# Kernel tuning notes

Measured on AMD Instinct MI355X. Metric: run time of the kernel, lower is better.

## Reference

```python
import jax, jax.numpy as jnp
import numpy as np

K_MASK = -2.3819763e+38
NUM_HEADS = 16
NUM_KV_HEADS = 8
FEATURES = 2048
HEAD_DIM = 128
WINDOW = 1024
SOFT_CAP = 50.0
B, T = 2, 2048


def apply_rope(inputs, positions, head_dim, max_wavelength=10000):
    # inputs: [B, T, N, H], positions: [B, T]
    fraction = 2 * jnp.arange(0, head_dim // 2) / head_dim
    timescale = max_wavelength ** fraction
    sinusoid_inp = positions[..., None] / timescale[None, None, :]  # [B,T,H/2]
    sinusoid_inp = sinusoid_inp[..., None, :]  # [B,T,1,H/2]
    sin = jnp.sin(sinusoid_inp)
    cos = jnp.cos(sinusoid_inp)
    first_half, second_half = jnp.split(inputs, 2, axis=-1)
    first_part = first_half * cos - second_half * sin
    second_part = second_half * cos + first_half * sin
    return jnp.concatenate([first_part, second_part], axis=-1).astype(inputs.dtype)


def setup_inputs() -> dict:
    key = jax.random.key(0)
    k1, k2, k3, k4 = jax.random.split(key, 4)
    std = 0.02
    x = jax.random.normal(k1, (B, T, FEATURES), dtype=jnp.float32)
    segment_pos = jnp.broadcast_to(jnp.arange(T, dtype=jnp.int32), (B, T))
    # causal prefill mask [B, T, T]
    attn_mask = jnp.broadcast_to(jnp.tril(jnp.ones((T, T), dtype=bool)), (B, T, T))
    wq = jax.random.normal(k2, (NUM_HEADS, FEATURES, HEAD_DIM), dtype=jnp.float32) * std
    wkv = jax.random.normal(k3, (2, NUM_KV_HEADS, FEATURES, HEAD_DIM), dtype=jnp.float32) * std
    wo = jax.random.normal(k4, (NUM_HEADS, HEAD_DIM, FEATURES), dtype=jnp.float32) * std
    return {"x": x, "segment_pos": segment_pos, "attn_mask": attn_mask,
            "wq": wq, "wkv": wkv, "wo": wo}


def reference(x, segment_pos, attn_mask, wq, wkv, wo):
    # Projections (GQA path: num_kv_heads != num_heads)
    q = jnp.einsum('BTD,NDH->BTNH', x, wq)              # [B,T,N,H]
    k = jnp.einsum('BSD,KDH->BSKH', x, wkv[0])          # [B,S,K,H]
    v = jnp.einsum('BSD,KDH->BSKH', x, wkv[1])          # [B,S,K,H]

    q = apply_rope(q, segment_pos, HEAD_DIM)
    q = q * HEAD_DIM ** (-0.5)
    k = apply_rope(k, segment_pos, HEAD_DIM)

    b, t, n, h = q.shape
    g = n // NUM_KV_HEADS
    qg = q.reshape(b, t, NUM_KV_HEADS, g, h)
    logits = jnp.einsum('BTKGH,BSKH->BTKGS', qg, k)
    s = logits.shape[-1]
    logits = logits.reshape(b, t, n, s)

    # soft cap
    logits = jnp.tanh(logits / SOFT_CAP) * SOFT_CAP

    # sliding-window mask combined with attn_mask
    cache_positions = jnp.arange(s)[None, None, :]
    sp = segment_pos[:, :, None]
    sliding_mask = (cache_positions >= sp - WINDOW + 1) & (cache_positions <= sp + WINDOW - 1)
    mask = sliding_mask & attn_mask  # [B,T,S]

    padded_logits = jnp.where(mask[:, :, None, :], logits, K_MASK)
    probs = jax.nn.softmax(padded_logits, axis=-1).astype(k.dtype)

    pg = probs.reshape(b, t, NUM_KV_HEADS, g, s)
    encoded = jnp.einsum('BTKGS,BSKH->BTKGH', pg, v).reshape(b, t, n, h)
    attn_output = jnp.einsum('BTNH,NHD->BTD', encoded, wo)
    return attn_output
```

## Files before the change

kernel.cpp:

```cpp
#include <hip/hip_runtime.h>

typedef unsigned short u16;
typedef unsigned int u32;
typedef __attribute__((ext_vector_type(8))) short bfx8;
typedef __attribute__((ext_vector_type(4))) float fx4;

static __device__ __forceinline__ float b2f(u16 u) {
    union { float f; u32 i; } c; c.i = ((u32)u) << 16; return c.f;
}
static __device__ __forceinline__ u16 f2b(float f) {
    union { float f; u32 i; } c; c.f = f;
    u32 r = c.i + 0x7FFFu + ((c.i >> 16) & 1u);
    return (u16)(r >> 16);
}
typedef const __attribute__((address_space(1))) unsigned int* gas1;
typedef __attribute__((address_space(3))) unsigned int* las3;
static __device__ __forceinline__ void gll16(const void* g, void* l) {
    __builtin_amdgcn_global_load_lds((gas1)g, (las3)l, 16, 0, 0);
}

__global__ __launch_bounds__(256) void k_convert_x(const float* __restrict__ x, u16* __restrict__ xb) {
    size_t i = ((size_t)blockIdx.x * 256 + threadIdx.x) * 8;
    float4 a = *(const float4*)(x + i);
    float4 b = *(const float4*)(x + i + 4);
    union { u16 e[8]; uint4 v; } o;
    o.e[0] = f2b(a.x); o.e[1] = f2b(a.y); o.e[2] = f2b(a.z); o.e[3] = f2b(a.w);
    o.e[4] = f2b(b.x); o.e[5] = f2b(b.y); o.e[6] = f2b(b.z); o.e[7] = f2b(b.w);
    *(uint4*)(xb + i) = o.v;
}

__global__ __launch_bounds__(256) void k_pack_w1(const float* __restrict__ wq, const float* __restrict__ wkv,
                                                 u16* __restrict__ wb1) {
    __shared__ float t[128 * 33];
    int ci = blockIdx.x;
    int k0 = blockIdx.y << 5;
    int c0 = ci << 7;
    const float* src;
    if (ci < 16)      src = wq  + (size_t)ci * 2048 * 128;
    else if (ci < 24) src = wkv + (size_t)(ci - 16) * 2048 * 128;
    else              src = wkv + (size_t)(8 + ci - 24) * 2048 * 128;
    int tid = threadIdx.x;
#pragma unroll
    for (int i = 0; i < 16; i++) {
        int idx = i * 256 + tid;
        int kk = idx >> 7, cc = idx & 127;
        t[cc * 33 + kk] = src[(size_t)(k0 + kk) * 128 + cc];
    }
    __syncthreads();
#pragma unroll
    for (int i = 0; i < 16; i++) {
        int idx = i * 256 + tid;
        int cc = idx >> 5, kk = idx & 31;
        wb1[(size_t)(c0 + cc) * 2048 + k0 + kk] = f2b(t[cc * 33 + kk]);
    }
}

__global__ __launch_bounds__(256) void k_pack_w2(const float* __restrict__ wo, u16* __restrict__ wb2) {
    __shared__ float t[128 * 33];
    int c0 = blockIdx.x << 7;
    int k0 = blockIdx.y << 5;
    int tid = threadIdx.x;
#pragma unroll
    for (int i = 0; i < 16; i++) {
        int idx = i * 256 + tid;
        int kk = idx >> 7, cc = idx & 127;
        t[cc * 33 + kk] = wo[(size_t)(k0 + kk) * 2048 + c0 + cc];
    }
    __syncthreads();
#pragma unroll
    for (int i = 0; i < 16; i++) {
        int idx = i * 256 + tid;
        int cc = idx >> 5, kk = idx & 31;
        wb2[(size_t)(c0 + cc) * 2048 + k0 + kk] = f2b(t[cc * 33 + kk]);
    }
}

template <int BM, int OUT_BF16>
__global__ __launch_bounds__(512, 2) void k_gemm256(const u16* __restrict__ A, const u16* __restrict__ Bt,
                                                    void* __restrict__ C, int M, int N, int K) {
    constexpr int MF = BM / 32;
    constexpr int NA = BM / 16;
    constexpr int FR = NA + 16;
    constexpr int LPW = FR / 8;
    __shared__ u16 lds[4 * FR * 512];

    int tid = threadIdx.x, wave = tid >> 6, lane = tid & 63;
    int quad = lane >> 4, l16 = lane & 15;
    int wm = wave >> 2, wn = wave & 3;

    int nwg = gridDim.x * gridDim.y;
    int bid = blockIdx.y * gridDim.x + blockIdx.x;
    int swz = (bid & 7) * (nwg >> 3) + (bid >> 3);
    int bx = swz % gridDim.x, by = swz / gridDim.x;
    int r0 = by * BM, c0 = bx << 8;

    fx4 zero = {0.f, 0.f, 0.f, 0.f};
    fx4 acc[MF][4];
#pragma unroll
    for (int m = 0; m < MF; m++)
#pragma unroll
        for (int n = 0; n < 4; n++) acc[m][n] = zero;

    const u16* gsrc[LPW];
#pragma unroll
    for (int j = 0; j < LPW; j++) {
        int fw = wave * LPW + j;
        gsrc[j] = (fw < NA ? A + (size_t)(r0 + fw * 16 + l16) * K
                           : Bt + (size_t)(c0 + (fw - NA) * 16 + l16) * K) + quad * 8;
    }
    u16* ldst = lds + wave * (LPW * 512);

    int NT = K >> 5;
#pragma unroll
    for (int p = 0; p < 3; p++)
#pragma unroll
        for (int j = 0; j < LPW; j++) gll16(gsrc[j] + p * 32, ldst + p * (FR * 512) + j * 512);

    for (int t = 0; t < NT; ++t) {
        int rem = NT - 1 - t;
        if (rem >= 2)      asm volatile("s_waitcnt vmcnt(%0)" : : "n"(2 * LPW) : "memory");
        else if (rem == 1) asm volatile("s_waitcnt vmcnt(%0)" : : "n"(LPW) : "memory");
        else               asm volatile("s_waitcnt vmcnt(0)" : : : "memory");
        __builtin_amdgcn_s_barrier();

        const u16* Fb = lds + (t & 3) * (FR * 512);
        const u16* Ab = Fb + wm * (MF * 512);
        const u16* Bb = Fb + (NA + wn * 4) * 512;
        bfx8 bf[4], af[4];
#pragma unroll
        for (int n = 0; n < 4; n++) bf[n] = *(const bfx8*)(Bb + n * 512 + lane * 8);
#pragma unroll
        for (int m = 0; m < 4; m++) af[m] = *(const bfx8*)(Ab + m * 512 + lane * 8);
        if (t + 3 < NT) {
            u16* dst = lds + ((t + 3) & 3) * (FR * 512) + wave * (LPW * 512);
#pragma unroll
            for (int j = 0; j < LPW; j++) gll16(gsrc[j] + (size_t)(t + 3) * 32, dst + j * 512);
        }
        __builtin_amdgcn_s_barrier();
        __builtin_amdgcn_s_setprio(1);
#pragma unroll
        for (int m = 0; m < 4; m++)
#pragma unroll
            for (int n = 0; n < 4; n++)
                acc[m][n] = __builtin_amdgcn_mfma_f32_16x16x32_bf16(af[m], bf[n], acc[m][n], 0, 0, 0);
        __builtin_amdgcn_s_setprio(0);
        if constexpr (MF == 8) {
            __builtin_amdgcn_s_barrier();
#pragma unroll
            for (int m = 0; m < 4; m++) af[m] = *(const bfx8*)(Ab + (4 + m) * 512 + lane * 8);
            __builtin_amdgcn_s_barrier();
            __builtin_amdgcn_s_setprio(1);
#pragma unroll
            for (int m = 0; m < 4; m++)
#pragma unroll
                for (int n = 0; n < 4; n++)
                    acc[4 + m][n] = __builtin_amdgcn_mfma_f32_16x16x32_bf16(af[m], bf[n], acc[4 + m][n], 0, 0, 0);
            __builtin_amdgcn_s_setprio(0);
        }
    }
#pragma unroll
    for (int m = 0; m < MF; m++)
#pragma unroll
        for (int n = 0; n < 4; n++) {
            int col = c0 + wn * 64 + n * 16 + l16;
#pragma unroll
            for (int r = 0; r < 4; r++) {
                int row = r0 + wm * (BM / 2) + m * 16 + quad * 4 + r;
                float v = acc[m][n][r];
                if (OUT_BF16) ((u16*)C)[(size_t)row * N + col] = f2b(v);
                else          ((float*)C)[(size_t)row * N + col] = v;
            }
        }
}

__global__ __launch_bounds__(256) void k_rope(const u16* __restrict__ qkv, u16* __restrict__ Qb,
                                              u16* __restrict__ Kb, u16* __restrict__ Vb) {
    __shared__ float sc[128];
    int bt = blockIdx.x;
    int b = bt >> 11, t = bt & 2047;
    const u16* row = qkv + (size_t)bt * 4096;
    int tid = threadIdx.x;
    float tf = (float)t;
    const float RS = 0.08838834764831845f;
    const float LT = 0.20762050593046f;
    if (tid < 64) {
        float ang = tf * exp2f(-LT * (float)tid);
        float s, c; sincosf(ang, &s, &c);
        sc[tid] = s; sc[tid + 64] = c;
    }
    __syncthreads();
#pragma unroll
    for (int i = 0; i < 4; i++) {
        int idx = tid + i * 256;
        int n = idx >> 6, hp = idx & 63;
        float x1 = b2f(row[n * 128 + hp]);
        float x2 = b2f(row[n * 128 + hp + 64]);
        float s = sc[hp], c = sc[hp + 64];
        size_t o = ((size_t)(b * 16 + n) * 2048 + t) * 128 + hp;
        Qb[o]      = f2b((x1 * c - x2 * s) * RS);
        Qb[o + 64] = f2b((x2 * c + x1 * s) * RS);
    }
#pragma unroll
    for (int i = 0; i < 2; i++) {
        int idx = tid + i * 256;
        int kh = idx >> 6, hp = idx & 63;
        float x1 = b2f(row[2048 + kh * 128 + hp]);
        float x2 = b2f(row[2048 + kh * 128 + hp + 64]);
        float s = sc[hp], c = sc[hp + 64];
        size_t o = ((size_t)(b * 8 + kh) * 2048 + t) * 128 + hp;
        Kb[o]      = f2b(x1 * c - x2 * s);
        Kb[o + 64] = f2b(x2 * c + x1 * s);
    }
#pragma unroll
    for (int i = 0; i < 4; i++) {
        int idx = tid + i * 256;
        int kh = idx >> 7, h = idx & 127;
        Vb[((size_t)(b * 8 + kh) * 2048 + t) * 128 + h] = row[3072 + idx];
    }
}

__global__ __launch_bounds__(256) void k_transpose_v(const u16* __restrict__ Vb, u16* __restrict__ Vt) {
    __shared__ u16 t[128 * 136];
    int bk = blockIdx.y;
    int t0 = blockIdx.x << 7;
    const u16* src = Vb + ((size_t)bk * 2048 + t0) * 128;
    u16* dst = Vt + (size_t)bk * 128 * 2048 + t0;
    int tid = threadIdx.x;
#pragma unroll
    for (int it = 0; it < 8; it++) {
        int ch = tid + it * 256;
        int tt = ch >> 4, c8 = (ch & 15) << 3;
        *(uint4*)(t + tt * 136 + c8) = *(const uint4*)(src + (size_t)tt * 128 + c8);
    }
    __syncthreads();
#pragma unroll
    for (int it = 0; it < 8; it++) {
        int ch = tid + it * 256;
        int h = ch >> 4, s8 = (ch & 15) << 3;
        union { uint4 v; u16 e[8]; } vv;
#pragma unroll
        for (int j = 0; j < 8; j++) vv.e[j] = t[(s8 + j) * 136 + h];
        *(uint4*)(dst + (size_t)h * 2048 + s8) = vv.v;
    }
}

__global__ __launch_bounds__(512, 4) void k_attn(const u16* __restrict__ Qb, const u16* __restrict__ Kb,
                                                 const u16* __restrict__ Vt, u16* __restrict__ enc) {
    __shared__ u16 Ks[2][16 * 512];
    __shared__ u16 Vs[2][16 * 512];
    __shared__ u16 Pl[8 * 1024];
    int t0 = blockIdx.x << 6;
    int kh = blockIdx.y, b = blockIdx.z;
    int tid = threadIdx.x, wave = tid >> 6, lane = tid & 63;
    int quad = lane >> 4, l16 = lane & 15;
    int n = (kh << 1) + (wave >> 2);
    int tw = t0 + ((wave & 3) << 4);
    const u16* Qp = Qb + (size_t)(b * 16 + n) * 2048 * 128;
    const u16* Kp = Kb + (size_t)(b * 8 + kh) * 2048 * 128;
    const u16* Vp = Vt + (size_t)(b * 8 + kh) * 128 * 2048;

    bfx8 aq[4];
#pragma unroll
    for (int kb = 0; kb < 4; kb++)
        aq[kb] = *(const bfx8*)(Qp + (size_t)(tw + l16) * 128 + kb * 32 + quad * 8);

    const u16* kgp[2]; const u16* vgp[2];
#pragma unroll
    for (int q = 0; q < 2; q++) {
        int f = wave * 2 + q;
        kgp[q] = Kp + (size_t)((f >> 2) * 16 + l16) * 128 + (f & 3) * 32 + quad * 8;
        vgp[q] = Vp + (size_t)((f >> 1) * 16 + l16) * 2048 + (f & 1) * 32 + quad * 8;
    }
    u16* Pw = Pl + wave * 1024;

    fx4 zero = {0.f, 0.f, 0.f, 0.f};
    fx4 o_acc[8];
#pragma unroll
    for (int hb = 0; hb < 8; hb++) o_acc[hb] = zero;
    float lsum[4] = {0.f, 0.f, 0.f, 0.f};

    const float C1 = 0.057707801635559f;
    const float C2 = 144.269504088896f;

    int s_lo = t0 - 1023; if (s_lo < 0) s_lo = 0;
    int ts0 = s_lo >> 6, ts1 = t0 >> 6;

#pragma unroll
    for (int q = 0; q < 2; q++) {
        int f = wave * 2 + q;
        gll16(kgp[q] + (size_t)(ts0 << 6) * 128, Ks[0] + f * 512);
        gll16(vgp[q] + (ts0 << 6), Vs[0] + f * 512);
    }

    for (int ts = ts0; ts <= ts1; ts++) {
        int cur = (ts - ts0) & 1;
        int s0 = ts << 6;
        __builtin_amdgcn_s_barrier();
        if (ts < ts1) {
            int s1 = (ts + 1) << 6;
#pragma unroll
            for (int q = 0; q < 2; q++) {
                int f = wave * 2 + q;
                gll16(kgp[q] + (size_t)s1 * 128, Ks[cur ^ 1] + f * 512);
                gll16(vgp[q] + s1, Vs[cur ^ 1] + f * 512);
            }
            asm volatile("s_waitcnt vmcnt(4)" : : : "memory");
        } else {
            asm volatile("s_waitcnt vmcnt(0)" : : : "memory");
        }
        __builtin_amdgcn_s_barrier();

        if (s0 <= tw + 15 && s0 + 63 >= tw - 1023) {
            const u16* Kc = Ks[cur];
            const u16* Vc = Vs[cur];
            bool full = (s0 + 63 <= tw) && (s0 >= tw - 1008);
            if (full) {
#pragma unroll
                for (int nb = 0; nb < 4; nb++) {
                    fx4 sacc = zero;
                    __builtin_amdgcn_s_setprio(1);
#pragma unroll
                    for (int kb = 0; kb < 4; kb++) {
                        bfx8 bk = *(const bfx8*)(Kc + (nb * 4 + kb) * 512 + lane * 8);
                        sacc = __builtin_amdgcn_mfma_f32_16x16x32_bf16(aq[kb], bk, sacc, 0, 0, 0);
                    }
                    __builtin_amdgcn_s_setprio(0);
                    int base0 = ((nb >> 1) * 64 + ((nb & 1) * 2 + (l16 >> 3)) * 16 + quad * 4) * 8 + (l16 & 7);
#pragma unroll
                    for (int r = 0; r < 4; r++) {
                        float u = __builtin_amdgcn_exp2f(sacc[r] * C1);
                        float p = __builtin_amdgcn_exp2f(-C2 * __builtin_amdgcn_rcpf(u + 1.f));
                        lsum[r] += p;
                        Pw[base0 + r * 8] = f2b(p);
                    }
                }
            } else {
#pragma unroll
                for (int nb = 0; nb < 4; nb++) {
                    int sb = s0 + (nb << 4);
                    int base0 = ((nb >> 1) * 64 + ((nb & 1) * 2 + (l16 >> 3)) * 16 + quad * 4) * 8 + (l16 & 7);
                    if (sb <= tw + 15 && sb + 15 >= tw - 1023) {
                        fx4 sacc = zero;
#pragma unroll
                        for (int kb = 0; kb < 4; kb++) {
                            bfx8 bk = *(const bfx8*)(Kc + (nb * 4 + kb) * 512 + lane * 8);
                            sacc = __builtin_amdgcn_mfma_f32_16x16x32_bf16(aq[kb], bk, sacc, 0, 0, 0);
                        }
                        int sg = sb + l16;
#pragma unroll
                        for (int r = 0; r < 4; r++) {
                            int tg = tw + quad * 4 + r;
                            float u = __builtin_amdgcn_exp2f(sacc[r] * C1);
                            float p = __builtin_amdgcn_exp2f(-C2 * __builtin_amdgcn_rcpf(u + 1.f));
                            p = (sg <= tg && sg >= tg - 1023) ? p : 0.f;
                            lsum[r] += p;
                            Pw[base0 + r * 8] = f2b(p);
                        }
                    } else {
#pragma unroll
                        for (int r = 0; r < 4; r++) Pw[base0 + r * 8] = 0;
                    }
                }
            }
            asm volatile("s_waitcnt lgkmcnt(0)" : : : "memory");
            __builtin_amdgcn_sched_barrier(0);
            bfx8 pf[2];
#pragma unroll
            for (int kk = 0; kk < 2; kk++)
                pf[kk] = *(const bfx8*)(Pw + kk * 512 + lane * 8);
            __builtin_amdgcn_s_setprio(1);
#pragma unroll
            for (int hb = 0; hb < 8; hb++)
#pragma unroll
                for (int kk = 0; kk < 2; kk++) {
                    bfx8 vf = *(const bfx8*)(Vc + (hb * 2 + kk) * 512 + lane * 8);
                    o_acc[hb] = __builtin_amdgcn_mfma_f32_16x16x32_bf16(pf[kk], vf, o_acc[hb], 0, 0, 0);
                }
            __builtin_amdgcn_s_setprio(0);
        }
    }
#pragma unroll
    for (int r = 0; r < 4; r++) {
#pragma unroll
        for (int off = 1; off < 16; off <<= 1)
            lsum[r] += __shfl_xor(lsum[r], off);
        lsum[r] = 1.0f / lsum[r];
    }
#pragma unroll
    for (int hb = 0; hb < 8; hb++) {
        int h = hb * 16 + l16;
#pragma unroll
        for (int r = 0; r < 4; r++) {
            int tg = tw + quad * 4 + r;
            enc[((size_t)(b * 2048 + tg) * 16 + n) * 128 + h] = f2b(o_acc[hb][r] * lsum[r]);
        }
    }
}

extern "C" void kernel_launch(void* const* d_in, const int* in_sizes, int n_in,
                              void* d_out, int out_size, void* d_ws, size_t ws_size,
                              hipStream_t stream) {
    const float* x   = (const float*)d_in[0];
    const float* wq  = (const float*)d_in[3];
    const float* wkv = (const float*)d_in[4];
    const float* wo  = (const float*)d_in[5];
    char* ws = (char*)d_ws;
    const size_t MiB = 1024 * 1024;
    u16* xb  = (u16*)(ws);
    u16* wb1 = (u16*)(ws + 16 * MiB);
    u16* qkv = (u16*)(ws + 32 * MiB);
    u16* Qb  = (u16*)(ws);
    u16* Kb  = (u16*)(ws + 16 * MiB);
    u16* Vb  = (u16*)(ws + 24 * MiB);
    u16* enc = (u16*)(ws + 32 * MiB);
    u16* wb2 = (u16*)(ws + 48 * MiB);
    u16* Vt  = (u16*)(ws + 56 * MiB);

    k_convert_x<<<4096, 256, 0, stream>>>(x, xb);
    k_pack_w1<<<dim3(32, 64), 256, 0, stream>>>(wq, wkv, wb1);
    k_gemm256<256, 1><<<dim3(16, 16), 512, 0, stream>>>(xb, wb1, qkv, 4096, 4096, 2048);
    k_rope<<<4096, 256, 0, stream>>>(qkv, Qb, Kb, Vb);
    k_transpose_v<<<dim3(16, 16), 256, 0, stream>>>(Vb, Vt);
    k_pack_w2<<<dim3(16, 64), 256, 0, stream>>>(wo, wb2);
    k_attn<<<dim3(32, 8, 2), 512, 0, stream>>>(Qb, Kb, Vt, enc);
    k_gemm256<128, 0><<<dim3(8, 32), 512, 0, stream>>>(enc, wb2, d_out, 4096, 2048, 2048);
}
```

Baseline: 357.5 us.

## Merge prep kernels, restructure GEMM pipeline to 8-phase double buffer, rope Q in place

Merges the x conversion and W1 packing into one launch. Merges rope, V transpose and Wo packing into another. Q is now roped in place inside the qkv buffer and read by attention with a 4096 stride, which removes the separate Qb and Vb copies, and Vt is staged in the output buffer. The GEMM changes from a 4-stage K=32 pipeline to a 2-stage K=64 double buffer with interleaved LDS-read/MFMA phases separated by barriers. The trade-offs are fewer launches and less traffic against a shallower prefetch depth, more barriers, and a strided Q read.

```diff
diff --git a/kernel.cpp b/kernel.cpp
--- a/kernel.cpp
+++ b/kernel.cpp
@@ -19,70 +19,53 @@
     __builtin_amdgcn_global_load_lds((gas1)g, (las3)l, 16, 0, 0);
 }
 
-__global__ __launch_bounds__(256) void k_convert_x(const float* __restrict__ x, u16* __restrict__ xb) {
-    size_t i = ((size_t)blockIdx.x * 256 + threadIdx.x) * 8;
-    float4 a = *(const float4*)(x + i);
-    float4 b = *(const float4*)(x + i + 4);
-    union { u16 e[8]; uint4 v; } o;
-    o.e[0] = f2b(a.x); o.e[1] = f2b(a.y); o.e[2] = f2b(a.z); o.e[3] = f2b(a.w);
-    o.e[4] = f2b(b.x); o.e[5] = f2b(b.y); o.e[6] = f2b(b.z); o.e[7] = f2b(b.w);
-    *(uint4*)(xb + i) = o.v;
-}
-
-__global__ __launch_bounds__(256) void k_pack_w1(const float* __restrict__ wq, const float* __restrict__ wkv,
-                                                 u16* __restrict__ wb1) {
+__global__ __launch_bounds__(256) void k_prep1(const float* __restrict__ x, u16* __restrict__ xb,
+                                               const float* __restrict__ wq, const float* __restrict__ wkv,
+                                               u16* __restrict__ wb1) {
     __shared__ float t[128 * 33];
-    int ci = blockIdx.x;
-    int k0 = blockIdx.y << 5;
+    int bid = blockIdx.x, tid = threadIdx.x;
+    if (bid < 4096) {
+        size_t i = ((size_t)bid * 256 + tid) * 8;
+        float4 a = *(const float4*)(x + i);
+        float4 b = *(const float4*)(x + i + 4);
+        union { u16 e[8]; uint4 v; } o;
+        o.e[0] = f2b(a.x); o.e[1] = f2b(a.y); o.e[2] = f2b(a.z); o.e[3] = f2b(a.w);
+        o.e[4] = f2b(b.x); o.e[5] = f2b(b.y); o.e[6] = f2b(b.z); o.e[7] = f2b(b.w);
+        *(uint4*)(xb + i) = o.v;
+        return;
+    }
+    int idx = bid - 4096;
+    int ci = idx & 31;
+    int k0 = (idx >> 5) << 5;
     int c0 = ci << 7;
     const float* src;
     if (ci < 16)      src = wq  + (size_t)ci * 2048 * 128;
     else if (ci < 24) src = wkv + (size_t)(ci - 16) * 2048 * 128;
     else              src = wkv + (size_t)(8 + ci - 24) * 2048 * 128;
-    int tid = threadIdx.x;
 #pragma unroll
     for (int i = 0; i < 16; i++) {
-        int idx = i * 256 + tid;
-        int kk = idx >> 7, cc = idx & 127;
+        int id2 = i * 256 + tid;
+        int kk = id2 >> 7, cc = id2 & 127;
         t[cc * 33 + kk] = src[(size_t)(k0 + kk) * 128 + cc];
     }
     __syncthreads();
 #pragma unroll
     for (int i = 0; i < 16; i++) {
-        int idx = i * 256 + tid;
-        int cc = idx >> 5, kk = idx & 31;
+        int id2 = i * 256 + tid;
+        int cc = id2 >> 5, kk = id2 & 31;
         wb1[(size_t)(c0 + cc) * 2048 + k0 + kk] = f2b(t[cc * 33 + kk]);
     }
 }
 
-__global__ __launch_bounds__(256) void k_pack_w2(const float* __restrict__ wo, u16* __restrict__ wb2) {
-    __shared__ float t[128 * 33];
-    int c0 = blockIdx.x << 7;
-    int k0 = blockIdx.y << 5;
-    int tid = threadIdx.x;
-#pragma unroll
-    for (int i = 0; i < 16; i++) {
-        int idx = i * 256 + tid;
-        int kk = idx >> 7, cc = idx & 127;
-        t[cc * 33 + kk] = wo[(size_t)(k0 + kk) * 2048 + c0 + cc];
-    }
-    __syncthreads();
-#pragma unroll
-    for (int i = 0; i < 16; i++) {
-        int idx = i * 256 + tid;
-        int cc = idx >> 5, kk = idx & 31;
-        wb2[(size_t)(c0 + cc) * 2048 + k0 + kk] = f2b(t[cc * 33 + kk]);
-    }
-}
-
 template <int BM, int OUT_BF16>
-__global__ __launch_bounds__(512, 2) void k_gemm256(const u16* __restrict__ A, const u16* __restrict__ Bt,
-                                                    void* __restrict__ C, int M, int N, int K) {
+__global__ __launch_bounds__(512, 2) void k_gemm8p(const u16* __restrict__ A, const u16* __restrict__ Bt,
+                                                   void* __restrict__ C, int M, int N, int K) {
     constexpr int MF = BM / 32;
-    constexpr int NA = BM / 16;
-    constexpr int FR = NA + 16;
+    constexpr int MH = MF / 2;
+    constexpr int AF = BM / 8;
+    constexpr int FR = AF + 32;
     constexpr int LPW = FR / 8;
-    __shared__ u16 lds[4 * FR * 512];
+    __shared__ u16 lds[2 * FR * 512];
 
     int tid = threadIdx.x, wave = tid >> 6, lane = tid & 63;
     int quad = lane >> 4, l16 = lane & 15;
@@ -105,59 +88,70 @@
 #pragma unroll
     for (int j = 0; j < LPW; j++) {
         int fw = wave * LPW + j;
-        gsrc[j] = (fw < NA ? A + (size_t)(r0 + fw * 16 + l16) * K
-                           : Bt + (size_t)(c0 + (fw - NA) * 16 + l16) * K) + quad * 8;
-    }
-    u16* ldst = lds + wave * (LPW * 512);
-
-    int NT = K >> 5;
-#pragma unroll
-    for (int p = 0; p < 3; p++)
-#pragma unroll
-        for (int j = 0; j < LPW; j++) gll16(gsrc[j] + p * 32, ldst + p * (FR * 512) + j * 512);
-
-    for (int t = 0; t < NT; ++t) {
-        int rem = NT - 1 - t;
-        if (rem >= 2)      asm volatile("s_waitcnt vmcnt(%0)" : : "n"(2 * LPW) : "memory");
-        else if (rem == 1) asm volatile("s_waitcnt vmcnt(%0)" : : "n"(LPW) : "memory");
-        else               asm volatile("s_waitcnt vmcnt(0)" : : : "memory");
-        __builtin_amdgcn_s_barrier();
-
-        const u16* Fb = lds + (t & 3) * (FR * 512);
-        const u16* Ab = Fb + wm * (MF * 512);
-        const u16* Bb = Fb + (NA + wn * 4) * 512;
-        bfx8 bf[4], af[4];
-#pragma unroll
-        for (int n = 0; n < 4; n++) bf[n] = *(const bfx8*)(Bb + n * 512 + lane * 8);
-#pragma unroll
-        for (int m = 0; m < 4; m++) af[m] = *(const bfx8*)(Ab + m * 512 + lane * 8);
-        if (t + 3 < NT) {
-            u16* dst = lds + ((t + 3) & 3) * (FR * 512) + wave * (LPW * 512);
-#pragma unroll
-            for (int j = 0; j < LPW; j++) gll16(gsrc[j] + (size_t)(t + 3) * 32, dst + j * 512);
-        }
-        __builtin_amdgcn_s_barrier();
-        __builtin_amdgcn_s_setprio(1);
-#pragma unroll
-        for (int m = 0; m < 4; m++)
-#pragma unroll
-            for (int n = 0; n < 4; n++)
-                acc[m][n] = __builtin_amdgcn_mfma_f32_16x16x32_bf16(af[m], bf[n], acc[m][n], 0, 0, 0);
-        __builtin_amdgcn_s_setprio(0);
-        if constexpr (MF == 8) {
-            __builtin_amdgcn_s_barrier();
-#pragma unroll
-            for (int m = 0; m < 4; m++) af[m] = *(const bfx8*)(Ab + (4 + m) * 512 + lane * 8);
-            __builtin_amdgcn_s_barrier();
-            __builtin_amdgcn_s_setprio(1);
-#pragma unroll
-            for (int m = 0; m < 4; m++)
-#pragma unroll
-                for (int n = 0; n < 4; n++)
-                    acc[4 + m][n] = __builtin_amdgcn_mfma_f32_16x16x32_bf16(af[m], bf[n], acc[4 + m][n], 0, 0, 0);
-            __builtin_amdgcn_s_setprio(0);
-        }
-    }
+        const u16* base;
+        if (fw < AF) base = A + (size_t)(r0 + (fw >> 1) * 16 + l16) * K;
+        else { int g = fw - AF; base = Bt + (size_t)(c0 + (g >> 1) * 16 + l16) * K; }
+        gsrc[j] = base + (fw & 1) * 32 + quad * 8;
+    }
+
+    int NT = K >> 6;
+#pragma unroll
+    for (int j = 0; j < LPW; j++) gll16(gsrc[j], lds + wave * (LPW * 512) + j * 512);
+    asm volatile("s_waitcnt vmcnt(0)" : : : "memory");
+    __builtin_amdgcn_s_barrier();
+
+    bfx8 ax[MH][2], bu[2][2], bv[2][2];
+
+#define MFMA_PH(AH, NB, BV)                                                                               \
+    __builtin_amdgcn_s_setprio(1);                                                                        \
+    _Pragma("unroll") for (int kk = 0; kk < 2; kk++)                                                      \
+    _Pragma("unroll") for (int m = 0; m < MH; m++)                                                        \
+    _Pragma("unroll") for (int n = 0; n < 2; n++)                                                         \
+        acc[(AH) * MH + m][(NB) * 2 + n] =                                                                \
+            __builtin_amdgcn_mfma_f32_16x16x32_bf16(ax[m][kk], BV[n][kk], acc[(AH) * MH + m][(NB) * 2 + n], 0, 0, 0); \
+    __builtin_amdgcn_s_setprio(0);
+
+    for (int T = 0; T < NT; ++T) {
+        const u16* buf = lds + (T & 1) * (FR * 512);
+        if (T + 1 < NT) {
+            u16* dst = lds + ((T + 1) & 1) * (FR * 512) + wave * (LPW * 512);
+#pragma unroll
+            for (int j = 0; j < LPW; j++) gll16(gsrc[j] + (size_t)(T + 1) * 64, dst + j * 512);
+        }
+#pragma unroll
+        for (int m = 0; m < MH; m++)
+#pragma unroll
+            for (int kk = 0; kk < 2; kk++)
+                ax[m][kk] = *(const bfx8*)(buf + (((wm * MF + m) << 1) + kk) * 512 + lane * 8);
+#pragma unroll
+        for (int n = 0; n < 2; n++)
+#pragma unroll
+            for (int kk = 0; kk < 2; kk++)
+                bu[n][kk] = *(const bfx8*)(buf + (AF + (((wn << 2) + n) << 1) + kk) * 512 + lane * 8);
+        __builtin_amdgcn_s_barrier();
+        MFMA_PH(0, 0, bu)
+        __builtin_amdgcn_s_barrier();
+#pragma unroll
+        for (int n = 0; n < 2; n++)
+#pragma unroll
+            for (int kk = 0; kk < 2; kk++)
+                bv[n][kk] = *(const bfx8*)(buf + (AF + (((wn << 2) + 2 + n) << 1) + kk) * 512 + lane * 8);
+        __builtin_amdgcn_s_barrier();
+        MFMA_PH(0, 1, bv)
+        __builtin_amdgcn_s_barrier();
+#pragma unroll
+        for (int m = 0; m < MH; m++)
+#pragma unroll
+            for (int kk = 0; kk < 2; kk++)
+                ax[m][kk] = *(const bfx8*)(buf + (((wm * MF + MH + m) << 1) + kk) * 512 + lane * 8);
+        __builtin_amdgcn_s_barrier();
+        MFMA_PH(1, 0, bu)
+        __builtin_amdgcn_s_barrier();
+        MFMA_PH(1, 1, bv)
+        asm volatile("s_waitcnt vmcnt(0)" : : : "memory");
+        __builtin_amdgcn_s_barrier();
+    }
+#undef MFMA_PH
 #pragma unroll
     for (int m = 0; m < MF; m++)
 #pragma unroll
@@ -173,78 +167,92 @@
         }
 }
 
-__global__ __launch_bounds__(256) void k_rope(const u16* __restrict__ qkv, u16* __restrict__ Qb,
-                                              u16* __restrict__ Kb, u16* __restrict__ Vb) {
-    __shared__ float sc[128];
-    int bt = blockIdx.x;
-    int b = bt >> 11, t = bt & 2047;
-    const u16* row = qkv + (size_t)bt * 4096;
-    int tid = threadIdx.x;
-    float tf = (float)t;
-    const float RS = 0.08838834764831845f;
-    const float LT = 0.20762050593046f;
-    if (tid < 64) {
-        float ang = tf * exp2f(-LT * (float)tid);
-        float s, c; sincosf(ang, &s, &c);
-        sc[tid] = s; sc[tid + 64] = c;
+__global__ __launch_bounds__(256) void k_mid(u16* __restrict__ qkv, u16* __restrict__ Kb,
+                                             u16* __restrict__ Vt,
+                                             const float* __restrict__ wo, u16* __restrict__ wb2) {
+    __shared__ __align__(16) char smem[128 * 136 * 2];
+    int bid = blockIdx.x, tid = threadIdx.x;
+    if (bid < 4096) {
+        float* sc = (float*)smem;
+        int b = bid >> 11, t = bid & 2047;
+        u16* row = qkv + (size_t)bid * 4096;
+        float tf = (float)t;
+        const float RS = 0.08838834764831845f;
+        const float LT = 0.20762050593046f;
+        if (tid < 64) {
+            float ang = tf * exp2f(-LT * (float)tid);
+            float s, c; sincosf(ang, &s, &c);
+            sc[tid] = s; sc[tid + 64] = c;
+        }
+        __syncthreads();
+#pragma unroll
+        for (int i = 0; i < 4; i++) {
+            int idx = tid + i * 256;
+            int n = idx >> 6, hp = idx & 63;
+            float x1 = b2f(row[n * 128 + hp]);
+            float x2 = b2f(row[n * 128 + hp + 64]);
+            float s = sc[hp], c = sc[hp + 64];
+            row[n * 128 + hp]      = f2b((x1 * c - x2 * s) * RS);
+            row[n * 128 + hp + 64] = f2b((x2 * c + x1 * s) * RS);
+        }
+#pragma unroll
+        for (int i = 0; i < 2; i++) {
+            int idx = tid + i * 256;
+            int kh = idx >> 6, hp = idx & 63;
+            float x1 = b2f(row[2048 + kh * 128 + hp]);
+            float x2 = b2f(row[2048 + kh * 128 + hp + 64]);
+            float s = sc[hp], c = sc[hp + 64];
+            size_t o = ((size_t)(b * 8 + kh) * 2048 + t) * 128 + hp;
+            Kb[o]      = f2b(x1 * c - x2 * s);
+            Kb[o + 64] = f2b(x2 * c + x1 * s);
+        }
+        return;
+    }
+    if (bid < 4352) {
+        u16* t = (u16*)smem;
+        int idx = bid - 4096;
+        int bk = idx >> 4;
+        int t0 = (idx & 15) << 7;
+        const u16* src = qkv + ((size_t)((bk >> 3) * 2048 + t0)) * 4096 + 3072 + (bk & 7) * 128;
+        u16* dst = Vt + (size_t)bk * 128 * 2048 + t0;
+#pragma unroll
+        for (int it = 0; it < 8; it++) {
+            int ch = tid + it * 256;
+            int tt = ch >> 4, c8 = (ch & 15) << 3;
+            *(uint4*)(t + tt * 136 + c8) = *(const uint4*)(src + (size_t)tt * 4096 + c8);
+        }
+        __syncthreads();
+#pragma unroll
+        for (int it = 0; it < 8; it++) {
+            int ch = tid + it * 256;
+            int h = ch >> 4, s8 = (ch & 15) << 3;
+            union { uint4 v; u16 e[8]; } vv;
+#pragma unroll
+            for (int j = 0; j < 8; j++) vv.e[j] = t[(s8 + j) * 136 + h];
+            *(uint4*)(dst + (size_t)h * 2048 + s8) = vv.v;
+        }
+        return;
+    }
+    float* t = (float*)smem;
+    int idx = bid - 4352;
+    int c0 = (idx & 15) << 7;
+    int k0 = (idx >> 4) << 5;
+#pragma unroll
+    for (int i = 0; i < 16; i++) {
+        int id2 = i * 256 + tid;
+        int kk = id2 >> 7, cc = id2 & 127;
+        t[cc * 33 + kk] = wo[(size_t)(k0 + kk) * 2048 + c0 + cc];
     }
     __syncthreads();
 #pragma unroll
-    for (int i = 0; i < 4; i++) {
-        int idx = tid + i * 256;
-        int n = idx >> 6, hp = idx & 63;
-        float x1 = b2f(row[n * 128 + hp]);
-        float x2 = b2f(row[n * 128 + hp + 64]);
-        float s = sc[hp], c = sc[hp + 64];
-        size_t o = ((size_t)(b * 16 + n) * 2048 + t) * 128 + hp;
-        Qb[o]      = f2b((x1 * c - x2 * s) * RS);
-        Qb[o + 64] = f2b((x2 * c + x1 * s) * RS);
-    }
-#pragma unroll
-    for (int i = 0; i < 2; i++) {
-        int idx = tid + i * 256;
-        int kh = idx >> 6, hp = idx & 63;
-        float x1 = b2f(row[2048 + kh * 128 + hp]);
-        float x2 = b2f(row[2048 + kh * 128 + hp + 64]);
-        float s = sc[hp], c = sc[hp + 64];
-        size_t o = ((size_t)(b * 8 + kh) * 2048 + t) * 128 + hp;
-        Kb[o]      = f2b(x1 * c - x2 * s);
-        Kb[o + 64] = f2b(x2 * c + x1 * s);
-    }
-#pragma unroll
-    for (int i = 0; i < 4; i++) {
-        int idx = tid + i * 256;
-        int kh = idx >> 7, h = idx & 127;
-        Vb[((size_t)(b * 8 + kh) * 2048 + t) * 128 + h] = row[3072 + idx];
-    }
-}
-
-__global__ __launch_bounds__(256) void k_transpose_v(const u16* __restrict__ Vb, u16* __restrict__ Vt) {
-    __shared__ u16 t[128 * 136];
-    int bk = blockIdx.y;
-    int t0 = blockIdx.x << 7;
-    const u16* src = Vb + ((size_t)bk * 2048 + t0) * 128;
-    u16* dst = Vt + (size_t)bk * 128 * 2048 + t0;
-    int tid = threadIdx.x;
-#pragma unroll
-    for (int it = 0; it < 8; it++) {
-        int ch = tid + it * 256;
-        int tt = ch >> 4, c8 = (ch & 15) << 3;
-        *(uint4*)(t + tt * 136 + c8) = *(const uint4*)(src + (size_t)tt * 128 + c8);
-    }
-    __syncthreads();
-#pragma unroll
-    for (int it = 0; it < 8; it++) {
-        int ch = tid + it * 256;
-        int h = ch >> 4, s8 = (ch & 15) << 3;
-        union { uint4 v; u16 e[8]; } vv;
-#pragma unroll
-        for (int j = 0; j < 8; j++) vv.e[j] = t[(s8 + j) * 136 + h];
-        *(uint4*)(dst + (size_t)h * 2048 + s8) = vv.v;
-    }
-}
-
-__global__ __launch_bounds__(512, 4) void k_attn(const u16* __restrict__ Qb, const u16* __restrict__ Kb,
+    for (int i = 0; i < 16; i++) {
+        int id2 = i * 256 + tid;
+        int cc = id2 >> 5, kk = id2 & 31;
+        wb2[(size_t)(c0 + cc) * 2048 + k0 + kk] = f2b(t[cc * 33 + kk]);
+    }
+}
+
+__global__ __launch_bounds__(512, 4) void k_attn(const u16* __restrict__ qkv, const u16* __restrict__ Kb,
                                                  const u16* __restrict__ Vt, u16* __restrict__ enc) {
     __shared__ u16 Ks[2][16 * 512];
     __shared__ u16 Vs[2][16 * 512];
@@ -255,14 +263,14 @@
     int quad = lane >> 4, l16 = lane & 15;
     int n = (kh << 1) + (wave >> 2);
     int tw = t0 + ((wave & 3) << 4);
-    const u16* Qp = Qb + (size_t)(b * 16 + n) * 2048 * 128;
+    const u16* Qp = qkv + (size_t)b * 2048 * 4096 + n * 128;
     const u16* Kp = Kb + (size_t)(b * 8 + kh) * 2048 * 128;
     const u16* Vp = Vt + (size_t)(b * 8 + kh) * 128 * 2048;
 
     bfx8 aq[4];
 #pragma unroll
     for (int kb = 0; kb < 4; kb++)
-        aq[kb] = *(const bfx8*)(Qp + (size_t)(tw + l16) * 128 + kb * 32 + quad * 8);
+        aq[kb] = *(const bfx8*)(Qp + (size_t)(tw + l16) * 4096 + kb * 32 + quad * 8);
 
     const u16* kgp[2]; const u16* vgp[2];
 #pragma unroll
@@ -409,19 +417,14 @@
     u16* xb  = (u16*)(ws);
     u16* wb1 = (u16*)(ws + 16 * MiB);
     u16* qkv = (u16*)(ws + 32 * MiB);
-    u16* Qb  = (u16*)(ws);
-    u16* Kb  = (u16*)(ws + 16 * MiB);
-    u16* Vb  = (u16*)(ws + 24 * MiB);
-    u16* enc = (u16*)(ws + 32 * MiB);
-    u16* wb2 = (u16*)(ws + 48 * MiB);
-    u16* Vt  = (u16*)(ws + 56 * MiB);
-
-    k_convert_x<<<4096, 256, 0, stream>>>(x, xb);
-    k_pack_w1<<<dim3(32, 64), 256, 0, stream>>>(wq, wkv, wb1);
-    k_gemm256<256, 1><<<dim3(16, 16), 512, 0, stream>>>(xb, wb1, qkv, 4096, 4096, 2048);
-    k_rope<<<4096, 256, 0, stream>>>(qkv, Qb, Kb, Vb);
-    k_transpose_v<<<dim3(16, 16), 256, 0, stream>>>(Vb, Vt);
-    k_pack_w2<<<dim3(16, 64), 256, 0, stream>>>(wo, wb2);
-    k_attn<<<dim3(32, 8, 2), 512, 0, stream>>>(Qb, Kb, Vt, enc);
-    k_gemm256<128, 0><<<dim3(8, 32), 512, 0, stream>>>(enc, wb2, d_out, 4096, 2048, 2048);
-}
+    u16* Kb  = (u16*)(ws);
+    u16* wb2 = (u16*)(ws + 8 * MiB);
+    u16* enc = (u16*)(ws + 16 * MiB);
+    u16* Vt  = (u16*)d_out;
+
+    k_prep1<<<6144, 256, 0, stream>>>(x, xb, wq, wkv, wb1);
+    k_gemm8p<256, 1><<<dim3(16, 16), 512, 0, stream>>>(xb, wb1, qkv, 4096, 4096, 2048);
+    k_mid<<<5376, 256, 0, stream>>>(qkv, Kb, Vt, wo, wb2);
+    k_attn<<<dim3(32, 8, 2), 512, 0, stream>>>(qkv, Kb, Vt, enc);
+    k_gemm8p<128, 0><<<dim3(8, 32), 512, 0, stream>>>(enc, wb2, d_out, 4096, 2048, 2048);
+}
```

Measured after the change: 365.9 us. 1.02x slower.
